# Performance work log

Hardware: AMD Instinct MI355X
Metric: run time of the kernel (lower is better)

The kernel has to match this reference:

```python
import jax, jax.numpy as jnp
import numpy as np

TOP_K = 2


def setup_inputs() -> dict:
    key = jax.random.key(0)
    k1, k2, k3, k4 = jax.random.split(key, 4)
    B, S, H, I, E = 2, 1024, 2048, 1408, 8
    hidden_states = jax.random.normal(k1, (B, S, H), dtype=jnp.float32)
    gate_w = jax.random.normal(k2, (E, H), dtype=jnp.float32) * (1.0 / np.sqrt(H))
    # stacked expert weights: gate_up_proj [E, 2I, H], down_proj [E, H, I] (torch Linear [out,in])
    w1 = jax.random.normal(k3, (E, 2 * I, H), dtype=jnp.float32) * (1.0 / np.sqrt(H))
    w2 = jax.random.normal(k4, (E, H, I), dtype=jnp.float32) * (1.0 / np.sqrt(I))
    return {"hidden_states": hidden_states, "gate_w": gate_w, "w1": w1, "w2": w2}


def reference(hidden_states, gate_w, w1, w2):
    B, S, H = hidden_states.shape
    E = gate_w.shape[0]
    T = B * S
    x = hidden_states.reshape(T, H)

    # --- gating: softmax -> top-k -> renormalize ---
    logits = jnp.einsum('th,eh->te', x, gate_w)            # [T, E]
    probs = jax.nn.softmax(logits, axis=-1)
    topw, sel = jax.lax.top_k(probs, TOP_K)                # [T, K]
    topw = topw / jnp.sum(topw, axis=-1, keepdims=True)

    # combine weights: [T, E], zero for unselected experts (equivalent to
    # dispatch/permute + per-token routing-weight scale + unpermute + sum)
    combine = jnp.zeros((T, E), dtype=x.dtype).at[
        jnp.arange(T)[:, None], sel].add(topw)

    # --- grouped expert FFN (computed densely per expert) ---
    gate_up = jnp.einsum('th,eoh->eto', x, w1)             # [E, T, 2I]
    g, u = jnp.split(gate_up, 2, axis=-1)
    act = jax.nn.silu(g) * u                               # SiluAndMul, [E, T, I]
    expert_out = jnp.einsum('eti,ehi->eth', act, w2)       # [E, T, H]

    # --- combine ---
    out = jnp.einsum('eth,te->th', expert_out, combine)    # [T, H]
    return out.reshape(B, S, H)
```

## Files before the change

kernel.cpp:

```cpp
#include <hip/hip_runtime.h>
#include <hip/hip_bf16.h>
#include <math.h>

#define T_TOK 2048
#define H_DIM 2048
#define I_DIM 1408
#define E_NUM 8
#define I2    2816

typedef __attribute__((ext_vector_type(8))) short short8;
typedef __attribute__((ext_vector_type(4))) float floatx4;
typedef __attribute__((ext_vector_type(8))) unsigned short bf16x8;
typedef __attribute__((ext_vector_type(4))) unsigned short bf16x4;
typedef unsigned short u16;

__device__ __forceinline__ u16 f2bf(float x) {
    unsigned u = __builtin_bit_cast(unsigned, x);
    return (u16)((u + 0x7FFFu + ((u >> 16) & 1u)) >> 16);
}

__device__ __forceinline__ bf16x8 pack8(float4 a, float4 b) {
    bf16x8 o;
    o[0] = f2bf(a.x); o[1] = f2bf(a.y); o[2] = f2bf(a.z); o[3] = f2bf(a.w);
    o[4] = f2bf(b.x); o[5] = f2bf(b.y); o[6] = f2bf(b.z); o[7] = f2bf(b.w);
    return o;
}

__device__ __forceinline__ floatx4 mfma16(short8 a, short8 b, floatx4 c) {
    return __builtin_amdgcn_mfma_f32_16x16x32_bf16(a, b, c, 0, 0, 0);
}

__device__ __forceinline__ void gload16(const u16* g, u16* l) {
    __builtin_amdgcn_global_load_lds(
        (const __attribute__((address_space(1))) unsigned int*)g,
        (__attribute__((address_space(3))) unsigned int*)l, 16, 0, 0);
}

__global__ void moe_gating(const float* __restrict__ x, const float* __restrict__ gw,
                           u16* __restrict__ xb, float* __restrict__ wts,
                           int* __restrict__ counts, int* __restrict__ entries) {
    const int lane = threadIdx.x & 63;
    const int wv   = threadIdx.x >> 6;
    const int t    = blockIdx.x * 4 + wv;
    float acc[E_NUM];
#pragma unroll
    for (int e = 0; e < E_NUM; ++e) acc[e] = 0.f;
    const float4* xr = (const float4*)(x + (size_t)t * H_DIM);
    u16* xo = xb + (size_t)t * H_DIM;
#pragma unroll
    for (int j = 0; j < 8; ++j) {
        float4 xv = xr[lane + 64 * j];
        bf16x4 xw;
        xw[0] = f2bf(xv.x); xw[1] = f2bf(xv.y); xw[2] = f2bf(xv.z); xw[3] = f2bf(xv.w);
        *(bf16x4*)(xo + (lane + 64 * j) * 4) = xw;
#pragma unroll
        for (int e = 0; e < E_NUM; ++e) {
            float4 g = ((const float4*)(gw + (size_t)e * H_DIM))[lane + 64 * j];
            acc[e] += xv.x * g.x + xv.y * g.y + xv.z * g.z + xv.w * g.w;
        }
    }
#pragma unroll
    for (int off = 32; off > 0; off >>= 1)
#pragma unroll
        for (int e = 0; e < E_NUM; ++e) acc[e] += __shfl_xor(acc[e], off, 64);

    if (lane == 0) {
        int a = 0; float la = acc[0];
        for (int e = 1; e < E_NUM; ++e) if (acc[e] > la) { la = acc[e]; a = e; }
        int b = (a == 0) ? 1 : 0; float lb = acc[b];
        for (int e = 0; e < E_NUM; ++e)
            if (e != a && acc[e] > lb) { lb = acc[e]; b = e; }
        float wa = 1.f / (1.f + expf(lb - la));
        wts[t * 2 + 0] = wa;
        wts[t * 2 + 1] = 1.f - wa;
        int p0 = atomicAdd(&counts[a], 1); entries[a * T_TOK + p0] = t * 2;
        int p1 = atomicAdd(&counts[b], 1); entries[b * T_TOK + p1] = t * 2 + 1;
    }
}

__global__ __launch_bounds__(256)
void moe_mfma1(const u16* __restrict__ xb, const float* __restrict__ w1,
               const int* __restrict__ counts, const int* __restrict__ entries,
               u16* __restrict__ act) {
    const int bid = blockIdx.x;
    const int e   = bid & 7;
    const int rem = bid >> 3;
    const int tn  = rem >> 4;
    const int tm  = rem & 15;
    const int ne  = counts[e];
    if (tm * 128 >= ne) return;

    __shared__ __align__(16) u16 As[128 * 64];
    __shared__ __align__(16) u16 Bg[64 * 64];
    __shared__ __align__(16) u16 Bu[64 * 64];
    __shared__ int rowv[128];

    const int tid = threadIdx.x;
    if (tid < 128) {
        int r = tm * 128 + tid;
        rowv[tid] = (r < ne) ? entries[(size_t)e * T_TOK + r] : -1;
    }
    __syncthreads();

    const u16* asrc[4]; int ad[4];
#pragma unroll
    for (int q = 0; q < 4; ++q) {
        int i = q * 256 + tid;
        int row = i >> 3, pc = i & 7;
        int lc = pc ^ (row & 7);
        int v = rowv[row];
        int tok = (v < 0) ? 0 : (v >> 1);
        asrc[q] = xb + (size_t)tok * H_DIM + lc * 8;
        ad[q] = i * 8;
    }
    const int brow = tid >> 2;
    const int bc16 = (tid & 3) * 16;
    const float* gsrc = w1 + ((size_t)e * I2 + tn * 64 + brow) * H_DIM + bc16;
    const float* usrc = gsrc + (size_t)I_DIM * H_DIM;
    const int lc0 = (tid & 3) * 2;
    u16* bgd0 = Bg + brow * 64 + ((lc0    ) ^ (brow & 7)) * 8;
    u16* bgd1 = Bg + brow * 64 + ((lc0 + 1) ^ (brow & 7)) * 8;
    u16* bud0 = Bu + brow * 64 + ((lc0    ) ^ (brow & 7)) * 8;
    u16* bud1 = Bu + brow * 64 + ((lc0 + 1) ^ (brow & 7)) * 8;

    const int lane = tid & 63, wid = tid >> 6;
    const int wm = wid & 1, wn = wid >> 1;

    floatx4 accG[4][2], accU[4][2];
    const floatx4 z4 = {0.f, 0.f, 0.f, 0.f};
#pragma unroll
    for (int mi = 0; mi < 4; ++mi)
#pragma unroll
        for (int ni = 0; ni < 2; ++ni) { accG[mi][ni] = z4; accU[mi][ni] = z4; }

    int aoff[4][2], boff[2][2];
#pragma unroll
    for (int mi = 0; mi < 4; ++mi) {
        int m = wm * 64 + mi * 16 + (lane & 15);
#pragma unroll
        for (int kk = 0; kk < 2; ++kk)
            aoff[mi][kk] = m * 64 + (((kk * 4 + (lane >> 4)) ^ (m & 7)) * 8);
    }
#pragma unroll
    for (int ni = 0; ni < 2; ++ni) {
        int n = wn * 32 + ni * 16 + (lane & 15);
#pragma unroll
        for (int kk = 0; kk < 2; ++kk)
            boff[ni][kk] = n * 64 + (((kk * 4 + (lane >> 4)) ^ (n & 7)) * 8);
    }

#pragma unroll 1
    for (int k0 = 0; k0 < H_DIM; k0 += 64) {
#pragma unroll
        for (int q = 0; q < 4; ++q) gload16(asrc[q] + k0, As + ad[q]);
        {
            const float4* g4 = (const float4*)(gsrc + k0);
            const float4* u4 = (const float4*)(usrc + k0);
            float4 a0 = g4[0], a1 = g4[1], a2 = g4[2], a3 = g4[3];
            float4 b0 = u4[0], b1 = u4[1], b2 = u4[2], b3 = u4[3];
            *(bf16x8*)bgd0 = pack8(a0, a1);
            *(bf16x8*)bgd1 = pack8(a2, a3);
            *(bf16x8*)bud0 = pack8(b0, b1);
            *(bf16x8*)bud1 = pack8(b2, b3);
        }
        __syncthreads();
#pragma unroll
        for (int kk = 0; kk < 2; ++kk) {
            short8 a[4], g2[2], u2[2];
#pragma unroll
            for (int mi = 0; mi < 4; ++mi) a[mi] = *(const short8*)(As + aoff[mi][kk]);
#pragma unroll
            for (int ni = 0; ni < 2; ++ni) {
                g2[ni] = *(const short8*)(Bg + boff[ni][kk]);
                u2[ni] = *(const short8*)(Bu + boff[ni][kk]);
            }
#pragma unroll
            for (int mi = 0; mi < 4; ++mi)
#pragma unroll
                for (int ni = 0; ni < 2; ++ni) {
                    accG[mi][ni] = mfma16(a[mi], g2[ni], accG[mi][ni]);
                    accU[mi][ni] = mfma16(a[mi], u2[ni], accU[mi][ni]);
                }
        }
        __syncthreads();
    }

    const int obase = tn * 64 + wn * 32;
#pragma unroll
    for (int mi = 0; mi < 4; ++mi)
#pragma unroll
        for (int ni = 0; ni < 2; ++ni)
#pragma unroll
            for (int r = 0; r < 4; ++r) {
                int row = wm * 64 + mi * 16 + (lane >> 4) * 4 + r;
                int v = rowv[row];
                if (v < 0) continue;
                float g = accG[mi][ni][r], u = accU[mi][ni][r];
                float s = g / (1.f + expf(-g)) * u;
                act[(size_t)v * I_DIM + obase + ni * 16 + (lane & 15)] = f2bf(s);
            }
}

__global__ __launch_bounds__(256)
void moe_mfma2(const u16* __restrict__ act, const float* __restrict__ w2,
               const int* __restrict__ counts, const int* __restrict__ entries,
               const float* __restrict__ wts, float* __restrict__ out) {
    const int bid = blockIdx.x;
    const int e   = bid & 7;
    const int rem = bid >> 3;
    const int tn  = rem >> 4;
    const int tm  = rem & 15;
    const int ne  = counts[e];
    if (tm * 128 >= ne) return;

    __shared__ __align__(16) u16 As[128 * 64];
    __shared__ __align__(16) u16 Bs[128 * 64];
    __shared__ int   rowv[128];
    __shared__ int   rowt[128];
    __shared__ float roww[128];

    const int tid = threadIdx.x;
    if (tid < 128) {
        int r = tm * 128 + tid;
        int v = (r < ne) ? entries[(size_t)e * T_TOK + r] : -1;
        rowv[tid] = v;
        rowt[tid] = (v < 0) ? 0 : (v >> 1);
        roww[tid] = (v < 0) ? 0.f : wts[v];
    }
    __syncthreads();

    const u16* asrc[4]; int ad[4];
#pragma unroll
    for (int q = 0; q < 4; ++q) {
        int i = q * 256 + tid;
        int row = i >> 3, pc = i & 7;
        int lc = pc ^ (row & 7);
        int v = rowv[row]; if (v < 0) v = 0;
        asrc[q] = act + (size_t)v * I_DIM + lc * 8;
        ad[q] = i * 8;
    }
    const int brow = tid >> 1;
    const int bc32 = (tid & 1) * 32;
    const float* bsrc = w2 + ((size_t)e * H_DIM + tn * 128 + brow) * I_DIM + bc32;
    const int lcb = (tid & 1) * 4;
    u16* bd[4];
#pragma unroll
    for (int j = 0; j < 4; ++j)
        bd[j] = Bs + brow * 64 + (((lcb + j) ^ (brow & 7)) * 8);

    const int lane = tid & 63, wid = tid >> 6;
    const int wm = wid & 1, wn = wid >> 1;

    floatx4 acc[4][4];
    const floatx4 z4 = {0.f, 0.f, 0.f, 0.f};
#pragma unroll
    for (int mi = 0; mi < 4; ++mi)
#pragma unroll
        for (int ni = 0; ni < 4; ++ni) acc[mi][ni] = z4;

    int aoff[4][2], boff[4][2];
#pragma unroll
    for (int mi = 0; mi < 4; ++mi) {
        int m = wm * 64 + mi * 16 + (lane & 15);
#pragma unroll
        for (int kk = 0; kk < 2; ++kk)
            aoff[mi][kk] = m * 64 + (((kk * 4 + (lane >> 4)) ^ (m & 7)) * 8);
    }
#pragma unroll
    for (int ni = 0; ni < 4; ++ni) {
        int n = wn * 64 + ni * 16 + (lane & 15);
#pragma unroll
        for (int kk = 0; kk < 2; ++kk)
            boff[ni][kk] = n * 64 + (((kk * 4 + (lane >> 4)) ^ (n & 7)) * 8);
    }

#pragma unroll 1
    for (int k0 = 0; k0 < I_DIM; k0 += 64) {
#pragma unroll
        for (int q = 0; q < 4; ++q) gload16(asrc[q] + k0, As + ad[q]);
        {
            const float4* b4 = (const float4*)(bsrc + k0);
            float4 t0 = b4[0], t1 = b4[1], t2 = b4[2], t3 = b4[3];
            float4 t4 = b4[4], t5 = b4[5], t6 = b4[6], t7 = b4[7];
            *(bf16x8*)bd[0] = pack8(t0, t1);
            *(bf16x8*)bd[1] = pack8(t2, t3);
            *(bf16x8*)bd[2] = pack8(t4, t5);
            *(bf16x8*)bd[3] = pack8(t6, t7);
        }
        __syncthreads();
#pragma unroll
        for (int kk = 0; kk < 2; ++kk) {
            short8 a[4], b[4];
#pragma unroll
            for (int mi = 0; mi < 4; ++mi) a[mi] = *(const short8*)(As + aoff[mi][kk]);
#pragma unroll
            for (int ni = 0; ni < 4; ++ni) b[ni] = *(const short8*)(Bs + boff[ni][kk]);
#pragma unroll
            for (int mi = 0; mi < 4; ++mi)
#pragma unroll
                for (int ni = 0; ni < 4; ++ni)
                    acc[mi][ni] = mfma16(a[mi], b[ni], acc[mi][ni]);
        }
        __syncthreads();
    }

    const int hbase = tn * 128 + wn * 64;
#pragma unroll
    for (int mi = 0; mi < 4; ++mi)
#pragma unroll
        for (int ni = 0; ni < 4; ++ni)
#pragma unroll
            for (int r = 0; r < 4; ++r) {
                int row = wm * 64 + mi * 16 + (lane >> 4) * 4 + r;
                if (rowv[row] < 0) continue;
                atomicAdd(out + (size_t)rowt[row] * H_DIM + hbase + ni * 16 + (lane & 15),
                          roww[row] * acc[mi][ni][r]);
            }
}

extern "C" void kernel_launch(void* const* d_in, const int* in_sizes, int n_in,
                              void* d_out, int out_size, void* d_ws, size_t ws_size,
                              hipStream_t stream) {
    const float* x  = (const float*)d_in[0];
    const float* gw = (const float*)d_in[1];
    const float* w1 = (const float*)d_in[2];
    const float* w2 = (const float*)d_in[3];
    float* out = (float*)d_out;

    char* ws = (char*)d_ws;
    int*   counts  = (int*)ws;
    int*   entries = (int*)(ws + 256);
    float* wts     = (float*)(ws + 256 + 65536);
    u16* xb  = (u16*)(ws + 131072);
    u16* act = xb + (size_t)T_TOK * H_DIM;

    (void)hipMemsetAsync(counts, 0, 256, stream);
    (void)hipMemsetAsync(out, 0, (size_t)T_TOK * H_DIM * sizeof(float), stream);

    moe_gating<<<T_TOK / 4, 256, 0, stream>>>(x, gw, xb, wts, counts, entries);
    moe_mfma1<<<dim3(22 * 16 * E_NUM), 256, 0, stream>>>(xb, w1, counts, entries, act);
    moe_mfma2<<<dim3(16 * 16 * E_NUM), 256, 0, stream>>>(act, w2, counts, entries, wts, out);
}
```

Baseline: 650.0 us.

## Pre-convert expert weights to bf16 and replace atomic output accumulation with slot-and-combine

Each call, when the workspace is large enough, the fp32 expert weights are first converted to bf16 by a separate grid-stride kernel. New GEMM kernels then stream bf16 tiles straight into LDS with direct 16-byte loads, instead of converting fp32 weights inside each tile. The down-projection writes each routed token's weighted result to its own slot row, and a final combine kernel adds the two slots per token. This removes the output memset and the atomic accumulation. The cost is an extra full pass over both weight tensors each call and a large workspace; if the workspace is too small, the old fp32 path runs instead.

Result: faster. 568.0 us (-12.6%).

```diff
diff --git a/kernel.cpp b/kernel.cpp
--- a/kernel.cpp
+++ b/kernel.cpp
@@ -79,9 +79,253 @@
 }
 
 __global__ __launch_bounds__(256)
-void moe_mfma1(const u16* __restrict__ xb, const float* __restrict__ w1,
-               const int* __restrict__ counts, const int* __restrict__ entries,
-               u16* __restrict__ act) {
+void cvt_bf16(const float* __restrict__ src, u16* __restrict__ dst, long n8) {
+    const float4* s4 = (const float4*)src;
+    const long stride = (long)gridDim.x * 256;
+    for (long i = (long)blockIdx.x * 256 + threadIdx.x; i < n8; i += stride) {
+        float4 a = s4[2 * i], b = s4[2 * i + 1];
+        *(bf16x8*)(dst + (size_t)i * 8) = pack8(a, b);
+    }
+}
+
+__global__ __launch_bounds__(256)
+void moe_mfma1_pre(const u16* __restrict__ xb, const u16* __restrict__ w1b,
+                   const int* __restrict__ counts, const int* __restrict__ entries,
+                   u16* __restrict__ act) {
+    const int bid = blockIdx.x;
+    const int e   = bid & 7;
+    const int rem = bid >> 3;
+    const int tn  = rem >> 4;
+    const int tm  = rem & 15;
+    const int ne  = counts[e];
+    if (tm * 128 >= ne) return;
+
+    __shared__ __align__(16) u16 As[128 * 64];
+    __shared__ __align__(16) u16 Bg[64 * 64];
+    __shared__ __align__(16) u16 Bu[64 * 64];
+    __shared__ int rowv[128];
+
+    const int tid = threadIdx.x;
+    if (tid < 128) {
+        int r = tm * 128 + tid;
+        rowv[tid] = (r < ne) ? entries[(size_t)e * T_TOK + r] : -1;
+    }
+    __syncthreads();
+
+    const u16* asrc[4]; int ad[4];
+#pragma unroll
+    for (int q = 0; q < 4; ++q) {
+        int i = q * 256 + tid;
+        int row = i >> 3, pc = i & 7;
+        int lc = pc ^ (row & 7);
+        int v = rowv[row];
+        int tok = (v < 0) ? 0 : (v >> 1);
+        asrc[q] = xb + (size_t)tok * H_DIM + lc * 8;
+        ad[q] = i * 8;
+    }
+    const u16* gsrc[2]; const u16* usrc[2]; int bd2[2];
+#pragma unroll
+    for (int q = 0; q < 2; ++q) {
+        int i = q * 256 + tid;
+        int row = i >> 3, pc = i & 7;
+        int lc = pc ^ (row & 7);
+        size_t off = ((size_t)e * I2 + tn * 64 + row) * H_DIM + lc * 8;
+        gsrc[q] = w1b + off;
+        usrc[q] = w1b + off + (size_t)I_DIM * H_DIM;
+        bd2[q] = i * 8;
+    }
+
+    const int lane = tid & 63, wid = tid >> 6;
+    const int wm = wid & 1, wn = wid >> 1;
+
+    floatx4 accG[4][2], accU[4][2];
+    const floatx4 z4 = {0.f, 0.f, 0.f, 0.f};
+#pragma unroll
+    for (int mi = 0; mi < 4; ++mi)
+#pragma unroll
+        for (int ni = 0; ni < 2; ++ni) { accG[mi][ni] = z4; accU[mi][ni] = z4; }
+
+    int aoff[4][2], boff[2][2];
+#pragma unroll
+    for (int mi = 0; mi < 4; ++mi) {
+        int m = wm * 64 + mi * 16 + (lane & 15);
+#pragma unroll
+        for (int kk = 0; kk < 2; ++kk)
+            aoff[mi][kk] = m * 64 + (((kk * 4 + (lane >> 4)) ^ (m & 7)) * 8);
+    }
+#pragma unroll
+    for (int ni = 0; ni < 2; ++ni) {
+        int n = wn * 32 + ni * 16 + (lane & 15);
+#pragma unroll
+        for (int kk = 0; kk < 2; ++kk)
+            boff[ni][kk] = n * 64 + (((kk * 4 + (lane >> 4)) ^ (n & 7)) * 8);
+    }
+
+#pragma unroll 1
+    for (int k0 = 0; k0 < H_DIM; k0 += 64) {
+#pragma unroll
+        for (int q = 0; q < 4; ++q) gload16(asrc[q] + k0, As + ad[q]);
+#pragma unroll
+        for (int q = 0; q < 2; ++q) {
+            gload16(gsrc[q] + k0, Bg + bd2[q]);
+            gload16(usrc[q] + k0, Bu + bd2[q]);
+        }
+        __syncthreads();
+#pragma unroll
+        for (int kk = 0; kk < 2; ++kk) {
+            short8 a[4], g2[2], u2[2];
+#pragma unroll
+            for (int mi = 0; mi < 4; ++mi) a[mi] = *(const short8*)(As + aoff[mi][kk]);
+#pragma unroll
+            for (int ni = 0; ni < 2; ++ni) {
+                g2[ni] = *(const short8*)(Bg + boff[ni][kk]);
+                u2[ni] = *(const short8*)(Bu + boff[ni][kk]);
+            }
+#pragma unroll
+            for (int mi = 0; mi < 4; ++mi)
+#pragma unroll
+                for (int ni = 0; ni < 2; ++ni) {
+                    accG[mi][ni] = mfma16(a[mi], g2[ni], accG[mi][ni]);
+                    accU[mi][ni] = mfma16(a[mi], u2[ni], accU[mi][ni]);
+                }
+        }
+        __syncthreads();
+    }
+
+    const int obase = tn * 64 + wn * 32;
+#pragma unroll
+    for (int mi = 0; mi < 4; ++mi)
+#pragma unroll
+        for (int ni = 0; ni < 2; ++ni)
+#pragma unroll
+            for (int r = 0; r < 4; ++r) {
+                int row = wm * 64 + mi * 16 + (lane >> 4) * 4 + r;
+                int v = rowv[row];
+                if (v < 0) continue;
+                float g = accG[mi][ni][r], u = accU[mi][ni][r];
+                float s = g / (1.f + expf(-g)) * u;
+                act[(size_t)v * I_DIM + obase + ni * 16 + (lane & 15)] = f2bf(s);
+            }
+}
+
+__global__ __launch_bounds__(256)
+void moe_mfma2_pre(const u16* __restrict__ act, const u16* __restrict__ w2b,
+                   const int* __restrict__ counts, const int* __restrict__ entries,
+                   const float* __restrict__ wts, float* __restrict__ slot) {
+    const int bid = blockIdx.x;
+    const int e   = bid & 7;
+    const int rem = bid >> 3;
+    const int tn  = rem >> 4;
+    const int tm  = rem & 15;
+    const int ne  = counts[e];
+    if (tm * 128 >= ne) return;
+
+    __shared__ __align__(16) u16 As[128 * 64];
+    __shared__ __align__(16) u16 Bs[128 * 64];
+    __shared__ int   rowv[128];
+    __shared__ float roww[128];
+
+    const int tid = threadIdx.x;
+    if (tid < 128) {
+        int r = tm * 128 + tid;
+        int v = (r < ne) ? entries[(size_t)e * T_TOK + r] : -1;
+        rowv[tid] = v;
+        roww[tid] = (v < 0) ? 0.f : wts[v];
+    }
+    __syncthreads();
+
+    const u16* asrc[4]; const u16* bsrc[4]; int ad[4];
+#pragma unroll
+    for (int q = 0; q < 4; ++q) {
+        int i = q * 256 + tid;
+        int row = i >> 3, pc = i & 7;
+        int lc = pc ^ (row & 7);
+        int v = rowv[row]; if (v < 0) v = 0;
+        asrc[q] = act + (size_t)v * I_DIM + lc * 8;
+        bsrc[q] = w2b + ((size_t)e * H_DIM + tn * 128 + row) * I_DIM + lc * 8;
+        ad[q] = i * 8;
+    }
+
+    const int lane = tid & 63, wid = tid >> 6;
+    const int wm = wid & 1, wn = wid >> 1;
+
+    floatx4 acc[4][4];
+    const floatx4 z4 = {0.f, 0.f, 0.f, 0.f};
+#pragma unroll
+    for (int mi = 0; mi < 4; ++mi)
+#pragma unroll
+        for (int ni = 0; ni < 4; ++ni) acc[mi][ni] = z4;
+
+    int aoff[4][2], boff[4][2];
+#pragma unroll
+    for (int mi = 0; mi < 4; ++mi) {
+        int m = wm * 64 + mi * 16 + (lane & 15);
+#pragma unroll
+        for (int kk = 0; kk < 2; ++kk)
+            aoff[mi][kk] = m * 64 + (((kk * 4 + (lane >> 4)) ^ (m & 7)) * 8);
+    }
+#pragma unroll
+    for (int ni = 0; ni < 4; ++ni) {
+        int n = wn * 64 + ni * 16 + (lane & 15);
+#pragma unroll
+        for (int kk = 0; kk < 2; ++kk)
+            boff[ni][kk] = n * 64 + (((kk * 4 + (lane >> 4)) ^ (n & 7)) * 8);
+    }
+
+#pragma unroll 1
+    for (int k0 = 0; k0 < I_DIM; k0 += 64) {
+#pragma unroll
+        for (int q = 0; q < 4; ++q) {
+            gload16(asrc[q] + k0, As + ad[q]);
+            gload16(bsrc[q] + k0, Bs + ad[q]);
+        }
+        __syncthreads();
+#pragma unroll
+        for (int kk = 0; kk < 2; ++kk) {
+            short8 a[4], b[4];
+#pragma unroll
+            for (int mi = 0; mi < 4; ++mi) a[mi] = *(const short8*)(As + aoff[mi][kk]);
+#pragma unroll
+            for (int ni = 0; ni < 4; ++ni) b[ni] = *(const short8*)(Bs + boff[ni][kk]);
+#pragma unroll
+            for (int mi = 0; mi < 4; ++mi)
+#pragma unroll
+                for (int ni = 0; ni < 4; ++ni)
+                    acc[mi][ni] = mfma16(a[mi], b[ni], acc[mi][ni]);
+        }
+        __syncthreads();
+    }
+
+    const int hbase = tn * 128 + wn * 64;
+#pragma unroll
+    for (int mi = 0; mi < 4; ++mi)
+#pragma unroll
+        for (int ni = 0; ni < 4; ++ni)
+#pragma unroll
+            for (int r = 0; r < 4; ++r) {
+                int row = wm * 64 + mi * 16 + (lane >> 4) * 4 + r;
+                int v = rowv[row];
+                if (v < 0) continue;
+                slot[(size_t)v * H_DIM + hbase + ni * 16 + (lane & 15)] =
+                    roww[row] * acc[mi][ni][r];
+            }
+}
+
+__global__ __launch_bounds__(256)
+void moe_combine(const float* __restrict__ slot, float* __restrict__ out) {
+    int i = blockIdx.x * 256 + threadIdx.x;
+    int t = i >> 9, c = i & 511;
+    const float4* s4 = (const float4*)slot;
+    float4 a = s4[(size_t)(2 * t) * 512 + c];
+    float4 b = s4[(size_t)(2 * t + 1) * 512 + c];
+    float4 o; o.x = a.x + b.x; o.y = a.y + b.y; o.z = a.z + b.z; o.w = a.w + b.w;
+    ((float4*)out)[i] = o;
+}
+
+__global__ __launch_bounds__(256)
+void moe_mfma1_f32(const u16* __restrict__ xb, const float* __restrict__ w1,
+                   const int* __restrict__ counts, const int* __restrict__ entries,
+                   u16* __restrict__ act) {
     const int bid = blockIdx.x;
     const int e   = bid & 7;
     const int rem = bid >> 3;
@@ -202,9 +446,9 @@
 }
 
 __global__ __launch_bounds__(256)
-void moe_mfma2(const u16* __restrict__ act, const float* __restrict__ w2,
-               const int* __restrict__ counts, const int* __restrict__ entries,
-               const float* __restrict__ wts, float* __restrict__ out) {
+void moe_mfma2_f32(const u16* __restrict__ act, const float* __restrict__ w2,
+                   const int* __restrict__ counts, const int* __restrict__ entries,
+                   const float* __restrict__ wts, float* __restrict__ out) {
     const int bid = blockIdx.x;
     const int e   = bid & 7;
     const int rem = bid >> 3;
@@ -332,12 +576,29 @@
     int*   entries = (int*)(ws + 256);
     float* wts     = (float*)(ws + 256 + 65536);
     u16* xb  = (u16*)(ws + 131072);
-    u16* act = xb + (size_t)T_TOK * H_DIM;
+    u16* act = xb  + (size_t)T_TOK * H_DIM;
+    u16* w1b = act + (size_t)2 * T_TOK * I_DIM;
+    u16* w2b = w1b + (size_t)E_NUM * I2 * H_DIM;
+    float* slot = (float*)w1b;
+
+    const size_t need = 131072 + 2ull * ((size_t)T_TOK * H_DIM + 2ull * T_TOK * I_DIM +
+                                         (size_t)E_NUM * I2 * H_DIM +
+                                         (size_t)E_NUM * H_DIM * I_DIM);
+    const bool pre = (ws_size >= need);
 
     (void)hipMemsetAsync(counts, 0, 256, stream);
-    (void)hipMemsetAsync(out, 0, (size_t)T_TOK * H_DIM * sizeof(float), stream);
 
     moe_gating<<<T_TOK / 4, 256, 0, stream>>>(x, gw, xb, wts, counts, entries);
-    moe_mfma1<<<dim3(22 * 16 * E_NUM), 256, 0, stream>>>(xb, w1, counts, entries, act);
-    moe_mfma2<<<dim3(16 * 16 * E_NUM), 256, 0, stream>>>(act, w2, counts, entries, wts, out);
-}
+
+    if (pre) {
+        cvt_bf16<<<4096, 256, 0, stream>>>(w1, w1b, (long)E_NUM * I2 * H_DIM / 8);
+        cvt_bf16<<<4096, 256, 0, stream>>>(w2, w2b, (long)E_NUM * H_DIM * I_DIM / 8);
+        moe_mfma1_pre<<<22 * 16 * E_NUM, 256, 0, stream>>>(xb, w1b, counts, entries, act);
+        moe_mfma2_pre<<<16 * 16 * E_NUM, 256, 0, stream>>>(act, w2b, counts, entries, wts, slot);
+        moe_combine<<<T_TOK * H_DIM / 4 / 256, 256, 0, stream>>>(slot, out);
+    } else {
+        (void)hipMemsetAsync(out, 0, (size_t)T_TOK * H_DIM * sizeof(float), stream);
+        moe_mfma1_f32<<<22 * 16 * E_NUM, 256, 0, stream>>>(xb, w1, counts, entries, act);
+        moe_mfma2_f32<<<16 * 16 * E_NUM, 256, 0, stream>>>(act, w2, counts, entries, wts, out);
+    }
+}
```
